# Kernel tuning notes

Measured on AMD Instinct MI355X. Metric: run time of the kernel, lower is better.

## Reference

```python
import jax, jax.numpy as jnp
import numpy as np

B, T, C = 64, 256, 384
H, HD = 6, 64


def setup_inputs() -> dict:
    key = jax.random.key(0)
    ks = jax.random.split(key, 6)
    x = jax.random.normal(ks[0], (B, T, C), dtype=jnp.float32)
    s = 1.0 / np.sqrt(C)
    Wq = jax.random.normal(ks[1], (H, C, HD), dtype=jnp.float32) * s
    Wk = jax.random.normal(ks[2], (H, C, HD), dtype=jnp.float32) * s
    Wv = jax.random.normal(ks[3], (H, C, HD), dtype=jnp.float32) * s
    Wp = jax.random.normal(ks[4], (C, C), dtype=jnp.float32) * s
    bp = jnp.zeros((C,), dtype=jnp.float32)
    return {"x": x, "Wq": Wq, "Wk": Wk, "Wv": Wv, "Wp": Wp, "bp": bp}


def reference(x, Wq, Wk, Wv, Wp, bp):
    # per-head projections (no bias), vectorized over heads
    q = jnp.einsum('btc,hcd->bhtd', x, Wq)
    k = jnp.einsum('btc,hcd->bhtd', x, Wk)
    v = jnp.einsum('btc,hcd->bhtd', x, Wv)
    scale = HD ** (-0.5)
    scores = jnp.einsum('bhtd,bhsd->bhts', q, k) * scale  # [B,H,T,T]
    causal = jnp.tril(jnp.ones((T, T), dtype=bool))
    scores = jnp.where(causal, scores, -jnp.inf)
    wei = jax.nn.softmax(scores, axis=-1)  # dropout is identity in eval mode
    out = jnp.einsum('bhts,bhsd->bhtd', wei, v)
    out = out.transpose(0, 2, 1, 3).reshape(B, T, C)  # concat heads
    return out @ Wp.T + bp
```

## Files before the change

kernel.cpp:

```cpp
#include <hip/hip_runtime.h>
#include <hip/hip_bf16.h>
#include <cstdint>
#include <cstddef>

#define B_ 64
#define T_ 256
#define C_ 384
#define H_ 6
#define HD_ 64

using u16 = unsigned short;
typedef __attribute__((ext_vector_type(8))) short short8;
typedef __attribute__((ext_vector_type(4))) short short4_;
typedef __attribute__((ext_vector_type(4))) float f32x4;

__device__ __forceinline__ u16 f2bf(float f) {
    union { float f; uint32_t u; } x{f};
    uint32_t r = x.u + 0x7fffu + ((x.u >> 16) & 1u);
    return (u16)(r >> 16);
}

__global__ void k_prep(const float* __restrict__ x, const float* __restrict__ Wq,
                       const float* __restrict__ Wk, const float* __restrict__ Wv,
                       const float* __restrict__ Wp, u16* __restrict__ xb,
                       u16* __restrict__ wqkv, u16* __restrict__ wpb) {
    int bid = blockIdx.x;
    if (bid < 3072) {
        int i = (bid * 256 + threadIdx.x) * 8;
        const f32x4* p = (const f32x4*)(x + i);
        f32x4 a = p[0], b = p[1];
        short8 s;
        s[0] = (short)f2bf(a[0]); s[1] = (short)f2bf(a[1]);
        s[2] = (short)f2bf(a[2]); s[3] = (short)f2bf(a[3]);
        s[4] = (short)f2bf(b[0]); s[5] = (short)f2bf(b[1]);
        s[6] = (short)f2bf(b[2]); s[7] = (short)f2bf(b[3]);
        *(short8*)(xb + i) = s;
    } else if (bid < 3180) {
        __shared__ u16 Tt[64 * 65];
        int pb = bid - 3072;
        int which = pb / 36, rem = pb % 36;
        int h = rem / 6, cc0 = (rem % 6) * 64;
        const float* W = (which == 0) ? Wq : ((which == 1) ? Wk : Wv);
        int d = threadIdx.x & 63, cr0 = threadIdx.x >> 6;
#pragma unroll
        for (int p = 0; p < 16; ++p) {
            int cr = p * 4 + cr0;
            Tt[cr * 65 + d] = f2bf(W[(h * 384 + cc0 + cr) * 64 + d]);
        }
        __syncthreads();
        int ccl = threadIdx.x & 63, dl0 = threadIdx.x >> 6;
        int nbase = which * 384 + h * 64;
#pragma unroll
        for (int p = 0; p < 16; ++p) {
            int dl = p * 4 + dl0;
            wqkv[(size_t)(nbase + dl) * 384 + cc0 + ccl] = Tt[ccl * 65 + dl];
        }
    } else {
        int i = ((bid - 3180) * 256 + threadIdx.x) * 8;
        const f32x4* p = (const f32x4*)(Wp + i);
        f32x4 a = p[0], b = p[1];
        short8 s;
        s[0] = (short)f2bf(a[0]); s[1] = (short)f2bf(a[1]);
        s[2] = (short)f2bf(a[2]); s[3] = (short)f2bf(a[3]);
        s[4] = (short)f2bf(b[0]); s[5] = (short)f2bf(b[1]);
        s[6] = (short)f2bf(b[2]); s[7] = (short)f2bf(b[3]);
        *(short8*)(wpb + i) = s;
    }
}

template<int NROWS>
__device__ __forceinline__ void stage_rows(const u16* __restrict__ gbase, int ld,
                                           u16* lds_tile, int wid, int lane, int k0) {
#pragma unroll
    for (int i = 0; i < NROWS / 32; ++i) {
        int chunk = wid * (NROWS / 32) + i;
        int row = chunk * 8 + (lane >> 3);
        int pslot = lane & 7;
        const u16* gp = gbase + (size_t)row * ld + k0 + ((pslot ^ (row & 7)) << 3);
        u16* lp = lds_tile + chunk * 512;
        __builtin_amdgcn_global_load_lds((const __attribute__((address_space(1))) void*)gp,
                                         (__attribute__((address_space(3))) void*)lp, 16, 0, 0);
    }
}

__device__ __forceinline__ void stage_tile(const u16* __restrict__ gbase, int ld,
                                           u16* lds_tile, int wid, int lane, int k0) {
    stage_rows<128>(gbase, ld, lds_tile, wid, lane, k0);
}

__device__ __forceinline__ short8 read_frag(const u16* lds_tile, int row, int ks, int g) {
    int pslot = (ks * 4 + g) ^ (row & 7);
    return *(const short8*)&lds_tile[row * 64 + pslot * 8];
}

#define GEMM_PIPE_LOOP(NT)                                                        \
    int cur = 0;                                                                  \
    for (int t = 0; t < (NT); ++t) {                                              \
        if (t < (NT) - 1) {                                                       \
            stage_tile(Ag, 384, &lds[cur ^ 1][0], wid, lane, (t + 1) * 64);       \
            stage_tile(Bg, 384, &lds[cur ^ 1][8192], wid, lane, (t + 1) * 64);    \
            asm volatile("s_waitcnt vmcnt(8)" ::: "memory");                      \
        } else {                                                                  \
            asm volatile("s_waitcnt vmcnt(0)" ::: "memory");                      \
        }                                                                         \
        __builtin_amdgcn_s_barrier();                                             \
        __builtin_amdgcn_sched_barrier(0);                                        \
        const u16* A = &lds[cur][0];                                              \
        const u16* Bm = &lds[cur][8192];                                          \
        short8 af[2][4], bf[2][4];                                                \
        _Pragma("unroll")                                                         \
        for (int ks = 0; ks < 2; ++ks) {                                          \
            _Pragma("unroll")                                                     \
            for (int mf = 0; mf < 4; ++mf) af[ks][mf] = read_frag(A, wm * 64 + mf * 16 + c, ks, g); \
            _Pragma("unroll")                                                     \
            for (int nf = 0; nf < 4; ++nf) bf[ks][nf] = read_frag(Bm, wn * 64 + nf * 16 + c, ks, g); \
        }                                                                         \
        _Pragma("unroll")                                                         \
        for (int ks = 0; ks < 2; ++ks)                                            \
            _Pragma("unroll")                                                     \
            for (int mf = 0; mf < 4; ++mf)                                        \
                _Pragma("unroll")                                                 \
                for (int nf = 0; nf < 4; ++nf)                                    \
                    acc[mf][nf] = __builtin_amdgcn_mfma_f32_16x16x32_bf16(af[ks][mf], bf[ks][nf], acc[mf][nf], 0, 0, 0); \
        __builtin_amdgcn_sched_barrier(0);                                        \
        __builtin_amdgcn_s_barrier();                                             \
        cur ^= 1;                                                                 \
    }

__global__ __launch_bounds__(256, 2) void k_gemm_qkv(const u16* __restrict__ xb, const u16* __restrict__ wb,
                                                     u16* __restrict__ q, u16* __restrict__ k,
                                                     u16* __restrict__ v) {
    __shared__ alignas(16) u16 lds[2][16384];
    const int tid = threadIdx.x, lane = tid & 63, wid = tid >> 6;
    const int wm = wid >> 1, wn = wid & 1, g = lane >> 4, c = lane & 15;
    const int wg = blockIdx.x;
    const int xcd = wg & 7, q8 = wg >> 3;
    const int mj = (q8 / 9) * 8 + xcd;
    const int nk = q8 % 9;
    const int n0 = nk * 128, m0 = mj * 128;
    const u16* Ag = xb + (size_t)m0 * 384;
    const u16* Bg = wb + (size_t)n0 * 384;
    f32x4 acc[4][4] = {};
    stage_tile(Ag, 384, &lds[0][0], wid, lane, 0);
    stage_tile(Bg, 384, &lds[0][8192], wid, lane, 0);
    GEMM_PIPE_LOOP(6)
    const int which = n0 / 384;
    u16* dst = (which == 0) ? q : ((which == 1) ? k : v);
    const int h = ((n0 + wn * 64) % 384) / 64;
#pragma unroll
    for (int mf = 0; mf < 4; ++mf)
#pragma unroll
        for (int nf = 0; nf < 4; ++nf)
#pragma unroll
            for (int r = 0; r < 4; ++r) {
                int m = m0 + wm * 64 + mf * 16 + g * 4 + r;
                int d = nf * 16 + c;
                int b = m >> 8, t = m & 255;
                dst[((b * H_ + h) * T_ + t) * HD_ + d] = f2bf(acc[mf][nf][r]);
            }
}

__global__ __launch_bounds__(256, 2) void k_attn(const u16* __restrict__ q, const u16* __restrict__ k,
                                                 const u16* __restrict__ v, u16* __restrict__ ao) {
    __shared__ alignas(16) u16 Kl[2][64 * 64];
    __shared__ alignas(16) u16 Vt[2][64][72];
    const int tid = threadIdx.x, bh = blockIdx.x;
    const int lane = tid & 63, wid = tid >> 6;
    const int g = lane >> 4, c = lane & 15;
    const int bq = bh * 256;

    const int vd0 = (tid & 15) * 4;
    const int vs0 = (tid >> 4) * 4;
    const int kb0 = ((vs0 >> 5) << 5) | (((vs0 >> 2) & 3) << 3) | (((vs0 >> 4) & 1) << 2);

    short8 qB[4][2];
#pragma unroll
    for (int qf = 0; qf < 4; ++qf)
#pragma unroll
        for (int ks = 0; ks < 2; ++ks) {
            int t = (qf * 4 + wid) * 16 + c;
            qB[qf][ks] = *(const short8*)&q[(bq + t) * 64 + ks * 32 + g * 8];
        }
    float mrun[4], lrun[4];
#pragma unroll
    for (int i = 0; i < 4; ++i) { mrun[i] = -1e30f; lrun[i] = 0.f; }
    f32x4 o[4][4] = {};

    short4_ vv[4];
    stage_rows<64>(k + (size_t)(bq) * 64, 64, &Kl[0][0], wid, lane, 0);
#pragma unroll
    for (int i = 0; i < 4; ++i)
        vv[i] = *(const short4_*)&v[(size_t)(bq + vs0 + i) * 64 + vd0];
#pragma unroll
    for (int j = 0; j < 4; ++j) {
        short4_ w4;
#pragma unroll
        for (int i = 0; i < 4; ++i) w4[i] = vv[i][j];
        *(short4_*)&Vt[0][vd0 + j][kb0] = w4;
    }
    __syncthreads();

#pragma unroll
    for (int kt = 0; kt < 4; ++kt) {
        const int buf = kt & 1;
        if (kt < 3) {
            stage_rows<64>(k + (size_t)(bq + (kt + 1) * 64) * 64, 64, &Kl[buf ^ 1][0], wid, lane, 0);
#pragma unroll
            for (int i = 0; i < 4; ++i)
                vv[i] = *(const short4_*)&v[(size_t)(bq + (kt + 1) * 64 + vs0 + i) * 64 + vd0];
        }
        {
            f32x4 st[4][4] = {};
            __builtin_amdgcn_s_setprio(1);
#pragma unroll
            for (int ks = 0; ks < 2; ++ks) {
                short8 kA[4];
#pragma unroll
                for (int sf = 0; sf < 4; ++sf)
                    kA[sf] = read_frag(&Kl[buf][0], sf * 16 + c, ks, g);
#pragma unroll
                for (int sf = 0; sf < 4; ++sf)
#pragma unroll
                    for (int qf = kt; qf < 4; ++qf)
                        st[sf][qf] = __builtin_amdgcn_mfma_f32_16x16x32_bf16(kA[sf], qB[qf][ks], st[sf][qf], 0, 0, 0);
            }
            __builtin_amdgcn_s_setprio(0);
            float pm[4];
#pragma unroll
            for (int qf = kt; qf < 4; ++qf) pm[qf] = -1e30f;
#pragma unroll
            for (int sf = 0; sf < 4; ++sf)
#pragma unroll
                for (int qf = kt; qf < 4; ++qf)
#pragma unroll
                    for (int r = 0; r < 4; ++r) {
                        float val = st[sf][qf][r] * 0.125f;
                        if (qf == kt) {
                            if (sf * 16 + g * 4 + r > 16 * wid + c) val = -1e30f;
                        }
                        st[sf][qf][r] = val;
                        pm[qf] = fmaxf(pm[qf], val);
                    }
            float alpha[4];
#pragma unroll
            for (int qf = kt; qf < 4; ++qf) {
                pm[qf] = fmaxf(pm[qf], __shfl_xor(pm[qf], 16));
                pm[qf] = fmaxf(pm[qf], __shfl_xor(pm[qf], 32));
                float mnew = fmaxf(mrun[qf], pm[qf]);
                alpha[qf] = __expf(mrun[qf] - mnew);
                mrun[qf] = mnew;
            }
            short8 pA[4][2];
#pragma unroll
            for (int qf = kt; qf < 4; ++qf) {
                float ls = 0.f;
#pragma unroll
                for (int ks = 0; ks < 2; ++ks) {
                    short8 pa;
#pragma unroll
                    for (int half = 0; half < 2; ++half) {
                        f32x4 sv = st[2 * ks + half][qf];
#pragma unroll
                        for (int r = 0; r < 4; ++r) {
                            float p = __expf(sv[r] - mrun[qf]);
                            ls += p;
                            pa[half * 4 + r] = (short)f2bf(p);
                        }
                    }
                    pA[qf][ks] = pa;
                }
                ls += __shfl_xor(ls, 16);
                ls += __shfl_xor(ls, 32);
                lrun[qf] = lrun[qf] * alpha[qf] + ls;
            }
#pragma unroll
            for (int qf = kt; qf < 4; ++qf)
#pragma unroll
                for (int r = 0; r < 4; ++r) {
                    float aof = __shfl(alpha[qf], g * 4 + r);
#pragma unroll
                    for (int df = 0; df < 4; ++df)
                        o[qf][df][r] *= aof;
                }
            __builtin_amdgcn_s_setprio(1);
#pragma unroll
            for (int ks = 0; ks < 2; ++ks) {
                short8 vB[4];
#pragma unroll
                for (int df = 0; df < 4; ++df)
                    vB[df] = *(short8*)&Vt[buf][df * 16 + c][ks * 32 + g * 8];
#pragma unroll
                for (int qf = kt; qf < 4; ++qf)
#pragma unroll
                    for (int df = 0; df < 4; ++df)
                        o[qf][df] = __builtin_amdgcn_mfma_f32_16x16x32_bf16(pA[qf][ks], vB[df], o[qf][df], 0, 0, 0);
            }
            __builtin_amdgcn_s_setprio(0);
        }
        if (kt < 3) {
#pragma unroll
            for (int j = 0; j < 4; ++j) {
                short4_ w4;
#pragma unroll
                for (int i = 0; i < 4; ++i) w4[i] = vv[i][j];
                *(short4_*)&Vt[buf ^ 1][vd0 + j][kb0] = w4;
            }
        }
        __syncthreads();
    }
    const int bb = bh / H_, hh = bh % H_;
#pragma unroll
    for (int qf = 0; qf < 4; ++qf)
#pragma unroll
        for (int r = 0; r < 4; ++r) {
            float inv = 1.0f / __shfl(lrun[qf], g * 4 + r);
            int t = (qf * 4 + wid) * 16 + g * 4 + r;
#pragma unroll
            for (int df = 0; df < 4; ++df) {
                int d = df * 16 + c;
                ao[((size_t)(bb * T_ + t)) * C_ + hh * 64 + d] = f2bf(o[qf][df][r] * inv);
            }
        }
}

__global__ __launch_bounds__(256, 2) void k_gemm_proj(const u16* __restrict__ ab, const u16* __restrict__ wp,
                                                      const float* __restrict__ bp, float* __restrict__ out) {
    __shared__ alignas(16) u16 lds[2][16384];
    const int tid = threadIdx.x, lane = tid & 63, wid = tid >> 6;
    const int wm = wid >> 1, wn = wid & 1, g = lane >> 4, c = lane & 15;
    const int wg = blockIdx.x;
    const int xcd = wg & 7, q8 = wg >> 3;
    const int mj = (q8 / 3) * 8 + xcd;
    const int nk = q8 % 3;
    const int n0 = nk * 128, m0 = mj * 128;
    const u16* Ag = ab + (size_t)m0 * 384;
    const u16* Bg = wp + (size_t)n0 * 384;
    f32x4 acc[4][4] = {};
    stage_tile(Ag, 384, &lds[0][0], wid, lane, 0);
    stage_tile(Bg, 384, &lds[0][8192], wid, lane, 0);
    GEMM_PIPE_LOOP(6)
#pragma unroll
    for (int mf = 0; mf < 4; ++mf)
#pragma unroll
        for (int nf = 0; nf < 4; ++nf)
#pragma unroll
            for (int r = 0; r < 4; ++r) {
                int m = m0 + wm * 64 + mf * 16 + g * 4 + r;
                int n = n0 + wn * 64 + nf * 16 + c;
                out[(size_t)m * C_ + n] = acc[mf][nf][r] + bp[n];
            }
}


extern "C" void kernel_launch(void* const* d_in, const int* in_sizes, int n_in,
                              void* d_out, int out_size, void* d_ws, size_t ws_size,
                              hipStream_t stream) {
    const float* x  = (const float*)d_in[0];
    const float* Wq = (const float*)d_in[1];
    const float* Wk = (const float*)d_in[2];
    const float* Wv = (const float*)d_in[3];
    const float* Wp = (const float*)d_in[4];
    const float* bp = (const float*)d_in[5];
    float* out = (float*)d_out;

    char* ws = (char*)d_ws;
    u16* xb   = (u16*)(ws);
    u16* wqkv = (u16*)(ws + 12582912);
    u16* wpb  = (u16*)(ws + 13467648);
    u16* qb   = (u16*)(ws + 13762560);
    u16* kb   = (u16*)(ws + 26345472);
    u16* vb   = (u16*)(ws + 38928384);
    u16* ab   = (u16*)(ws + 51511296);

    k_prep<<<3252, 256, 0, stream>>>(x, Wq, Wk, Wv, Wp, xb, wqkv, wpb);
    k_gemm_qkv<<<1152, 256, 0, stream>>>(xb, wqkv, qb, kb, vb);
    k_attn<<<384, 256, 0, stream>>>(qb, kb, vb, ab);
    k_gemm_proj<<<384, 256, 0, stream>>>(ab, wpb, bp, out);
}
```

Measured before the change: 61.87 us.

## Switch QKV and projection GEMMs to single-buffered 256x128 tiles

Both GEMM kernels now compute 256x128 output tiles per block, with each wave owning a 64x128 strip, instead of 128x128 tiles on a 2x2 wave grid. The double-buffered prefetch pipeline is replaced by a single LDS buffer that is loaded and fully waited on each K step. The aim is more operand reuse per LDS fragment and fewer blocks, at the cost of no load/compute overlap, higher accumulator register pressure, and fewer blocks than CUs for the projection GEMM.

```diff
diff --git a/kernel.cpp b/kernel.cpp
--- a/kernel.cpp
+++ b/kernel.cpp
@@ -83,81 +83,66 @@
     }
 }
 
-__device__ __forceinline__ void stage_tile(const u16* __restrict__ gbase, int ld,
-                                           u16* lds_tile, int wid, int lane, int k0) {
-    stage_rows<128>(gbase, ld, lds_tile, wid, lane, k0);
-}
-
 __device__ __forceinline__ short8 read_frag(const u16* lds_tile, int row, int ks, int g) {
     int pslot = (ks * 4 + g) ^ (row & 7);
     return *(const short8*)&lds_tile[row * 64 + pslot * 8];
 }
 
-#define GEMM_PIPE_LOOP(NT)                                                        \
-    int cur = 0;                                                                  \
-    for (int t = 0; t < (NT); ++t) {                                              \
-        if (t < (NT) - 1) {                                                       \
-            stage_tile(Ag, 384, &lds[cur ^ 1][0], wid, lane, (t + 1) * 64);       \
-            stage_tile(Bg, 384, &lds[cur ^ 1][8192], wid, lane, (t + 1) * 64);    \
-            asm volatile("s_waitcnt vmcnt(8)" ::: "memory");                      \
-        } else {                                                                  \
-            asm volatile("s_waitcnt vmcnt(0)" ::: "memory");                      \
-        }                                                                         \
+#define GEMM_LOOP_256x128()                                                       \
+    for (int t = 0; t < 6; ++t) {                                                 \
+        stage_rows<256>(Ag, 384, &lds[0], wid, lane, t * 64);                     \
+        stage_rows<128>(Bg, 384, &lds[16384], wid, lane, t * 64);                 \
+        asm volatile("s_waitcnt vmcnt(0)" ::: "memory");                          \
         __builtin_amdgcn_s_barrier();                                             \
         __builtin_amdgcn_sched_barrier(0);                                        \
-        const u16* A = &lds[cur][0];                                              \
-        const u16* Bm = &lds[cur][8192];                                          \
-        short8 af[2][4], bf[2][4];                                                \
         _Pragma("unroll")                                                         \
         for (int ks = 0; ks < 2; ++ks) {                                          \
+            short8 af[4], bf[8];                                                  \
             _Pragma("unroll")                                                     \
-            for (int mf = 0; mf < 4; ++mf) af[ks][mf] = read_frag(A, wm * 64 + mf * 16 + c, ks, g); \
+            for (int mf = 0; mf < 4; ++mf) af[mf] = read_frag(&lds[0], wid * 64 + mf * 16 + c, ks, g); \
             _Pragma("unroll")                                                     \
-            for (int nf = 0; nf < 4; ++nf) bf[ks][nf] = read_frag(Bm, wn * 64 + nf * 16 + c, ks, g); \
-        }                                                                         \
-        _Pragma("unroll")                                                         \
-        for (int ks = 0; ks < 2; ++ks)                                            \
+            for (int nf = 0; nf < 8; ++nf) bf[nf] = read_frag(&lds[16384], nf * 16 + c, ks, g); \
             _Pragma("unroll")                                                     \
             for (int mf = 0; mf < 4; ++mf)                                        \
                 _Pragma("unroll")                                                 \
-                for (int nf = 0; nf < 4; ++nf)                                    \
-                    acc[mf][nf] = __builtin_amdgcn_mfma_f32_16x16x32_bf16(af[ks][mf], bf[ks][nf], acc[mf][nf], 0, 0, 0); \
+                for (int nf = 0; nf < 8; ++nf)                                    \
+                    acc[mf][nf] = __builtin_amdgcn_mfma_f32_16x16x32_bf16(af[mf], bf[nf], acc[mf][nf], 0, 0, 0); \
+        }                                                                         \
         __builtin_amdgcn_sched_barrier(0);                                        \
         __builtin_amdgcn_s_barrier();                                             \
-        cur ^= 1;                                                                 \
     }
 
 __global__ __launch_bounds__(256, 2) void k_gemm_qkv(const u16* __restrict__ xb, const u16* __restrict__ wb,
                                                      u16* __restrict__ q, u16* __restrict__ k,
                                                      u16* __restrict__ v) {
-    __shared__ alignas(16) u16 lds[2][16384];
+    __shared__ alignas(16) u16 lds[24576];
     const int tid = threadIdx.x, lane = tid & 63, wid = tid >> 6;
-    const int wm = wid >> 1, wn = wid & 1, g = lane >> 4, c = lane & 15;
+    const int g = lane >> 4, c = lane & 15;
     const int wg = blockIdx.x;
     const int xcd = wg & 7, q8 = wg >> 3;
     const int mj = (q8 / 9) * 8 + xcd;
     const int nk = q8 % 9;
-    const int n0 = nk * 128, m0 = mj * 128;
+    const int n0 = nk * 128, m0 = mj * 256;
     const u16* Ag = xb + (size_t)m0 * 384;
     const u16* Bg = wb + (size_t)n0 * 384;
-    f32x4 acc[4][4] = {};
-    stage_tile(Ag, 384, &lds[0][0], wid, lane, 0);
-    stage_tile(Bg, 384, &lds[0][8192], wid, lane, 0);
-    GEMM_PIPE_LOOP(6)
+    f32x4 acc[4][8] = {};
+    GEMM_LOOP_256x128()
     const int which = n0 / 384;
     u16* dst = (which == 0) ? q : ((which == 1) ? k : v);
-    const int h = ((n0 + wn * 64) % 384) / 64;
+    const int cbase = n0 % 384;
 #pragma unroll
     for (int mf = 0; mf < 4; ++mf)
 #pragma unroll
-        for (int nf = 0; nf < 4; ++nf)
+        for (int nf = 0; nf < 8; ++nf) {
+            int col = cbase + nf * 16 + c;
+            int h = col >> 6, d = col & 63;
 #pragma unroll
             for (int r = 0; r < 4; ++r) {
-                int m = m0 + wm * 64 + mf * 16 + g * 4 + r;
-                int d = nf * 16 + c;
+                int m = m0 + wid * 64 + mf * 16 + g * 4 + r;
                 int b = m >> 8, t = m & 255;
                 dst[((b * H_ + h) * T_ + t) * HD_ + d] = f2bf(acc[mf][nf][r]);
             }
+        }
 }
 
 __global__ __launch_bounds__(256, 2) void k_attn(const u16* __restrict__ q, const u16* __restrict__ k,
@@ -325,30 +310,30 @@
 
 __global__ __launch_bounds__(256, 2) void k_gemm_proj(const u16* __restrict__ ab, const u16* __restrict__ wp,
                                                       const float* __restrict__ bp, float* __restrict__ out) {
-    __shared__ alignas(16) u16 lds[2][16384];
+    __shared__ alignas(16) u16 lds[24576];
     const int tid = threadIdx.x, lane = tid & 63, wid = tid >> 6;
-    const int wm = wid >> 1, wn = wid & 1, g = lane >> 4, c = lane & 15;
+    const int g = lane >> 4, c = lane & 15;
     const int wg = blockIdx.x;
     const int xcd = wg & 7, q8 = wg >> 3;
     const int mj = (q8 / 3) * 8 + xcd;
     const int nk = q8 % 3;
-    const int n0 = nk * 128, m0 = mj * 128;
+    const int n0 = nk * 128, m0 = mj * 256;
     const u16* Ag = ab + (size_t)m0 * 384;
     const u16* Bg = wp + (size_t)n0 * 384;
-    f32x4 acc[4][4] = {};
-    stage_tile(Ag, 384, &lds[0][0], wid, lane, 0);
-    stage_tile(Bg, 384, &lds[0][8192], wid, lane, 0);
-    GEMM_PIPE_LOOP(6)
+    f32x4 acc[4][8] = {};
+    GEMM_LOOP_256x128()
 #pragma unroll
     for (int mf = 0; mf < 4; ++mf)
 #pragma unroll
-        for (int nf = 0; nf < 4; ++nf)
+        for (int nf = 0; nf < 8; ++nf) {
+            int n = n0 + nf * 16 + c;
+            float b = bp[n];
 #pragma unroll
             for (int r = 0; r < 4; ++r) {
-                int m = m0 + wm * 64 + mf * 16 + g * 4 + r;
-                int n = n0 + wn * 64 + nf * 16 + c;
-                out[(size_t)m * C_ + n] = acc[mf][nf][r] + bp[n];
-            }
+                int m = m0 + wid * 64 + mf * 16 + g * 4 + r;
+                out[(size_t)m * C_ + n] = acc[mf][nf][r] + b;
+            }
+        }
 }
 
 
@@ -373,7 +358,7 @@
     u16* ab   = (u16*)(ws + 51511296);
 
     k_prep<<<3252, 256, 0, stream>>>(x, Wq, Wk, Wv, Wp, xb, wqkv, wpb);
-    k_gemm_qkv<<<1152, 256, 0, stream>>>(xb, wqkv, qb, kb, vb);
+    k_gemm_qkv<<<576, 256, 0, stream>>>(xb, wqkv, qb, kb, vb);
     k_attn<<<384, 256, 0, stream>>>(qb, kb, vb, ab);
-    k_gemm_proj<<<384, 256, 0, stream>>>(ab, wpb, bp, out);
-}
+    k_gemm_proj<<<192, 256, 0, stream>>>(ab, wpb, bp, out);
+}
```

Result: slower. 69.49 us (+12.3%).

## Fuse fp32-to-bf16 conversion of x into the QKV GEMM loader

Applied to the files above, without the earlier changes.

Drops the separate pass that converts x to bf16 and writes it to workspace. The QKV GEMM now stages fp32 x tiles straight into LDS with 32-wide k-steps and converts fragments to bf16 as it reads them, on a reworked 12-step pipeline. This removes a 12.6 MB write and re-read plus part of the prep launch, at the cost of doubled A-tile bytes in LDS, conversion ALU work inside the GEMM loop, and more barriers per tile. Because every N-tile block re-reads x, global fp32 read traffic for the GEMM grows ninefold over the bf16 path, though most of it should hit cache.

```diff
diff --git a/kernel.cpp b/kernel.cpp
--- a/kernel.cpp
+++ b/kernel.cpp
@@ -20,25 +20,13 @@
     return (u16)(r >> 16);
 }
 
-__global__ void k_prep(const float* __restrict__ x, const float* __restrict__ Wq,
-                       const float* __restrict__ Wk, const float* __restrict__ Wv,
-                       const float* __restrict__ Wp, u16* __restrict__ xb,
-                       u16* __restrict__ wqkv, u16* __restrict__ wpb) {
+__global__ void k_prep_w(const float* __restrict__ Wq, const float* __restrict__ Wk,
+                         const float* __restrict__ Wv, const float* __restrict__ Wp,
+                         u16* __restrict__ wqkv, u16* __restrict__ wpb) {
     int bid = blockIdx.x;
-    if (bid < 3072) {
-        int i = (bid * 256 + threadIdx.x) * 8;
-        const f32x4* p = (const f32x4*)(x + i);
-        f32x4 a = p[0], b = p[1];
-        short8 s;
-        s[0] = (short)f2bf(a[0]); s[1] = (short)f2bf(a[1]);
-        s[2] = (short)f2bf(a[2]); s[3] = (short)f2bf(a[3]);
-        s[4] = (short)f2bf(b[0]); s[5] = (short)f2bf(b[1]);
-        s[6] = (short)f2bf(b[2]); s[7] = (short)f2bf(b[3]);
-        *(short8*)(xb + i) = s;
-    } else if (bid < 3180) {
+    if (bid < 108) {
         __shared__ u16 Tt[64 * 65];
-        int pb = bid - 3072;
-        int which = pb / 36, rem = pb % 36;
+        int which = bid / 36, rem = bid % 36;
         int h = rem / 6, cc0 = (rem % 6) * 64;
         const float* W = (which == 0) ? Wq : ((which == 1) ? Wk : Wv);
         int d = threadIdx.x & 63, cr0 = threadIdx.x >> 6;
@@ -56,7 +44,7 @@
             wqkv[(size_t)(nbase + dl) * 384 + cc0 + ccl] = Tt[ccl * 65 + dl];
         }
     } else {
-        int i = ((bid - 3180) * 256 + threadIdx.x) * 8;
+        int i = ((bid - 108) * 256 + threadIdx.x) * 8;
         const f32x4* p = (const f32x4*)(Wp + i);
         f32x4 a = p[0], b = p[1];
         short8 s;
@@ -91,6 +79,257 @@
 __device__ __forceinline__ short8 read_frag(const u16* lds_tile, int row, int ks, int g) {
     int pslot = (ks * 4 + g) ^ (row & 7);
     return *(const short8*)&lds_tile[row * 64 + pslot * 8];
+}
+
+__device__ __forceinline__ void stage_A32(const float* __restrict__ gbase,
+                                          u16* lds_tile, int wid, int lane, int k0) {
+#pragma unroll
+    for (int i = 0; i < 4; ++i) {
+        int chunk = wid * 4 + i;
+        int row = chunk * 8 + (lane >> 3);
+        int pslot = lane & 7;
+        const float* gp = gbase + (size_t)row * 384 + k0 + ((pslot ^ (row & 7)) << 2);
+        u16* lp = lds_tile + chunk * 512;
+        __builtin_amdgcn_global_load_lds((const __attribute__((address_space(1))) void*)gp,
+                                         (__attribute__((address_space(3))) void*)lp, 16, 0, 0);
+    }
+}
+
+__device__ __forceinline__ short8 read_fragA(const u16* tile, int row, int g) {
+    int s0 = (2 * g) ^ (row & 7);
+    int s1 = (2 * g + 1) ^ (row & 7);
+    f32x4 lo = *(const f32x4*)&tile[row * 64 + s0 * 8];
+    f32x4 hi = *(const f32x4*)&tile[row * 64 + s1 * 8];
+    short8 s;
+#pragma unroll
+    for (int e = 0; e < 4; ++e) {
+        s[e] = (short)f2bf(lo[e]);
+        s[4 + e] = (short)f2bf(hi[e]);
+    }
+    return s;
+}
+
+__global__ __launch_bounds__(256, 2) void k_gemm_qkv(const float* __restrict__ x, const u16* __restrict__ wb,
+                                                     u16* __restrict__ q, u16* __restrict__ k,
+                                                     u16* __restrict__ v) {
+    __shared__ alignas(16) u16 lds[32768];
+    const int tid = threadIdx.x, lane = tid & 63, wid = tid >> 6;
+    const int wm = wid >> 1, wn = wid & 1, g = lane >> 4, c = lane & 15;
+    const int wg = blockIdx.x;
+    const int xcd = wg & 7, q8 = wg >> 3;
+    const int mj = (q8 / 9) * 8 + xcd;
+    const int nk = q8 % 9;
+    const int n0 = nk * 128, m0 = mj * 128;
+    const float* Ag = x + (size_t)m0 * 384;
+    const u16* Bg = wb + (size_t)n0 * 384;
+    f32x4 acc[4][4] = {};
+
+    stage_A32(Ag, &lds[0], wid, lane, 0);
+    stage_rows<128>(Bg, 384, &lds[16384], wid, lane, 0);
+
+    for (int s = 0; s < 12; ++s) {
+        const int t = s >> 1, h = s & 1;
+        if (s < 11)
+            stage_A32(Ag, &lds[((s + 1) & 1) * 8192], wid, lane, (s + 1) * 32);
+        if (h == 0 && t < 5)
+            stage_rows<128>(Bg, 384, &lds[16384 + ((t + 1) & 1) * 8192], wid, lane, (t + 1) * 64);
+        if (s <= 9)       asm volatile("s_waitcnt vmcnt(8)" ::: "memory");
+        else if (s == 10) asm volatile("s_waitcnt vmcnt(4)" ::: "memory");
+        else              asm volatile("s_waitcnt vmcnt(0)" ::: "memory");
+        __builtin_amdgcn_s_barrier();
+        __builtin_amdgcn_sched_barrier(0);
+        const u16* A = &lds[(s & 1) * 8192];
+        const u16* Bm = &lds[16384 + (t & 1) * 8192];
+        short8 af[4], bf[4];
+#pragma unroll
+        for (int mf = 0; mf < 4; ++mf) af[mf] = read_fragA(A, wm * 64 + mf * 16 + c, g);
+#pragma unroll
+        for (int nf = 0; nf < 4; ++nf) bf[nf] = read_frag(Bm, wn * 64 + nf * 16 + c, h, g);
+#pragma unroll
+        for (int mf = 0; mf < 4; ++mf)
+#pragma unroll
+            for (int nf = 0; nf < 4; ++nf)
+                acc[mf][nf] = __builtin_amdgcn_mfma_f32_16x16x32_bf16(af[mf], bf[nf], acc[mf][nf], 0, 0, 0);
+        __builtin_amdgcn_sched_barrier(0);
+        __builtin_amdgcn_s_barrier();
+    }
+    const int which = n0 / 384;
+    u16* dst = (which == 0) ? q : ((which == 1) ? k : v);
+    const int h = ((n0 + wn * 64) % 384) / 64;
+#pragma unroll
+    for (int mf = 0; mf < 4; ++mf)
+#pragma unroll
+        for (int nf = 0; nf < 4; ++nf)
+#pragma unroll
+            for (int r = 0; r < 4; ++r) {
+                int m = m0 + wm * 64 + mf * 16 + g * 4 + r;
+                int d = nf * 16 + c;
+                int b = m >> 8, t = m & 255;
+                dst[((b * H_ + h) * T_ + t) * HD_ + d] = f2bf(acc[mf][nf][r]);
+            }
+}
+
+__global__ __launch_bounds__(256, 2) void k_attn(const u16* __restrict__ q, const u16* __restrict__ k,
+                                                 const u16* __restrict__ v, u16* __restrict__ ao) {
+    __shared__ alignas(16) u16 Kl[2][64 * 64];
+    __shared__ alignas(16) u16 Vt[2][64][72];
+    const int tid = threadIdx.x, bh = blockIdx.x;
+    const int lane = tid & 63, wid = tid >> 6;
+    const int g = lane >> 4, c = lane & 15;
+    const int bq = bh * 256;
+
+    const int vd0 = (tid & 15) * 4;
+    const int vs0 = (tid >> 4) * 4;
+    const int kb0 = ((vs0 >> 5) << 5) | (((vs0 >> 2) & 3) << 3) | (((vs0 >> 4) & 1) << 2);
+
+    short8 qB[4][2];
+#pragma unroll
+    for (int qf = 0; qf < 4; ++qf)
+#pragma unroll
+        for (int ks = 0; ks < 2; ++ks) {
+            int t = (qf * 4 + wid) * 16 + c;
+            qB[qf][ks] = *(const short8*)&q[(bq + t) * 64 + ks * 32 + g * 8];
+        }
+    float mrun[4], lrun[4];
+#pragma unroll
+    for (int i = 0; i < 4; ++i) { mrun[i] = -1e30f; lrun[i] = 0.f; }
+    f32x4 o[4][4] = {};
+
+    short4_ vv[4];
+    stage_rows<64>(k + (size_t)(bq) * 64, 64, &Kl[0][0], wid, lane, 0);
+#pragma unroll
+    for (int i = 0; i < 4; ++i)
+        vv[i] = *(const short4_*)&v[(size_t)(bq + vs0 + i) * 64 + vd0];
+#pragma unroll
+    for (int j = 0; j < 4; ++j) {
+        short4_ w4;
+#pragma unroll
+        for (int i = 0; i < 4; ++i) w4[i] = vv[i][j];
+        *(short4_*)&Vt[0][vd0 + j][kb0] = w4;
+    }
+    __syncthreads();
+
+#pragma unroll
+    for (int kt = 0; kt < 4; ++kt) {
+        const int buf = kt & 1;
+        if (kt < 3) {
+            stage_rows<64>(k + (size_t)(bq + (kt + 1) * 64) * 64, 64, &Kl[buf ^ 1][0], wid, lane, 0);
+#pragma unroll
+            for (int i = 0; i < 4; ++i)
+                vv[i] = *(const short4_*)&v[(size_t)(bq + (kt + 1) * 64 + vs0 + i) * 64 + vd0];
+        }
+        {
+            f32x4 st[4][4] = {};
+            __builtin_amdgcn_s_setprio(1);
+#pragma unroll
+            for (int ks = 0; ks < 2; ++ks) {
+                short8 kA[4];
+#pragma unroll
+                for (int sf = 0; sf < 4; ++sf)
+                    kA[sf] = read_frag(&Kl[buf][0], sf * 16 + c, ks, g);
+#pragma unroll
+                for (int sf = 0; sf < 4; ++sf)
+#pragma unroll
+                    for (int qf = kt; qf < 4; ++qf)
+                        st[sf][qf] = __builtin_amdgcn_mfma_f32_16x16x32_bf16(kA[sf], qB[qf][ks], st[sf][qf], 0, 0, 0);
+            }
+            __builtin_amdgcn_s_setprio(0);
+            float pm[4];
+#pragma unroll
+            for (int qf = kt; qf < 4; ++qf) pm[qf] = -1e30f;
+#pragma unroll
+            for (int sf = 0; sf < 4; ++sf)
+#pragma unroll
+                for (int qf = kt; qf < 4; ++qf)
+#pragma unroll
+                    for (int r = 0; r < 4; ++r) {
+                        float val = st[sf][qf][r] * 0.125f;
+                        if (qf == kt) {
+                            if (sf * 16 + g * 4 + r > 16 * wid + c) val = -1e30f;
+                        }
+                        st[sf][qf][r] = val;
+                        pm[qf] = fmaxf(pm[qf], val);
+                    }
+            float alpha[4];
+#pragma unroll
+            for (int qf = kt; qf < 4; ++qf) {
+                pm[qf] = fmaxf(pm[qf], __shfl_xor(pm[qf], 16));
+                pm[qf] = fmaxf(pm[qf], __shfl_xor(pm[qf], 32));
+                float mnew = fmaxf(mrun[qf], pm[qf]);
+                alpha[qf] = __expf(mrun[qf] - mnew);
+                mrun[qf] = mnew;
+            }
+            short8 pA[4][2];
+#pragma unroll
+            for (int qf = kt; qf < 4; ++qf) {
+                float ls = 0.f;
+#pragma unroll
+                for (int ks = 0; ks < 2; ++ks) {
+                    short8 pa;
+#pragma unroll
+                    for (int half = 0; half < 2; ++half) {
+                        f32x4 sv = st[2 * ks + half][qf];
+#pragma unroll
+                        for (int r = 0; r < 4; ++r) {
+                            float p = __expf(sv[r] - mrun[qf]);
+                            ls += p;
+                            pa[half * 4 + r] = (short)f2bf(p);
+                        }
+                    }
+                    pA[qf][ks] = pa;
+                }
+                ls += __shfl_xor(ls, 16);
+                ls += __shfl_xor(ls, 32);
+                lrun[qf] = lrun[qf] * alpha[qf] + ls;
+            }
+#pragma unroll
+            for (int qf = kt; qf < 4; ++qf)
+#pragma unroll
+                for (int r = 0; r < 4; ++r) {
+                    float aof = __shfl(alpha[qf], g * 4 + r);
+#pragma unroll
+                    for (int df = 0; df < 4; ++df)
+                        o[qf][df][r] *= aof;
+                }
+            __builtin_amdgcn_s_setprio(1);
+#pragma unroll
+            for (int ks = 0; ks < 2; ++ks) {
+                short8 vB[4];
+#pragma unroll
+                for (int df = 0; df < 4; ++df)
+                    vB[df] = *(short8*)&Vt[buf][df * 16 + c][ks * 32 + g * 8];
+#pragma unroll
+                for (int qf = kt; qf < 4; ++qf)
+#pragma unroll
+                    for (int df = 0; df < 4; ++df)
+                        o[qf][df] = __builtin_amdgcn_mfma_f32_16x16x32_bf16(pA[qf][ks], vB[df], o[qf][df], 0, 0, 0);
+            }
+            __builtin_amdgcn_s_setprio(0);
+        }
+        if (kt < 3) {
+#pragma unroll
+            for (int j = 0; j < 4; ++j) {
+                short4_ w4;
+#pragma unroll
+                for (int i = 0; i < 4; ++i) w4[i] = vv[i][j];
+                *(short4_*)&Vt[buf ^ 1][vd0 + j][kb0] = w4;
+            }
+        }
+        __syncthreads();
+    }
+    const int bb = bh / H_, hh = bh % H_;
+#pragma unroll
+    for (int qf = 0; qf < 4; ++qf)
+#pragma unroll
+        for (int r = 0; r < 4; ++r) {
+            float inv = 1.0f / __shfl(lrun[qf], g * 4 + r);
+            int t = (qf * 4 + wid) * 16 + g * 4 + r;
+#pragma unroll
+            for (int df = 0; df < 4; ++df) {
+                int d = df * 16 + c;
+                ao[((size_t)(bb * T_ + t)) * C_ + hh * 64 + d] = f2bf(o[qf][df][r] * inv);
+            }
+        }
 }
 
 #define GEMM_PIPE_LOOP(NT)                                                        \
@@ -127,202 +366,6 @@
         cur ^= 1;                                                                 \
     }
 
-__global__ __launch_bounds__(256, 2) void k_gemm_qkv(const u16* __restrict__ xb, const u16* __restrict__ wb,
-                                                     u16* __restrict__ q, u16* __restrict__ k,
-                                                     u16* __restrict__ v) {
-    __shared__ alignas(16) u16 lds[2][16384];
-    const int tid = threadIdx.x, lane = tid & 63, wid = tid >> 6;
-    const int wm = wid >> 1, wn = wid & 1, g = lane >> 4, c = lane & 15;
-    const int wg = blockIdx.x;
-    const int xcd = wg & 7, q8 = wg >> 3;
-    const int mj = (q8 / 9) * 8 + xcd;
-    const int nk = q8 % 9;
-    const int n0 = nk * 128, m0 = mj * 128;
-    const u16* Ag = xb + (size_t)m0 * 384;
-    const u16* Bg = wb + (size_t)n0 * 384;
-    f32x4 acc[4][4] = {};
-    stage_tile(Ag, 384, &lds[0][0], wid, lane, 0);
-    stage_tile(Bg, 384, &lds[0][8192], wid, lane, 0);
-    GEMM_PIPE_LOOP(6)
-    const int which = n0 / 384;
-    u16* dst = (which == 0) ? q : ((which == 1) ? k : v);
-    const int h = ((n0 + wn * 64) % 384) / 64;
-#pragma unroll
-    for (int mf = 0; mf < 4; ++mf)
-#pragma unroll
-        for (int nf = 0; nf < 4; ++nf)
-#pragma unroll
-            for (int r = 0; r < 4; ++r) {
-                int m = m0 + wm * 64 + mf * 16 + g * 4 + r;
-                int d = nf * 16 + c;
-                int b = m >> 8, t = m & 255;
-                dst[((b * H_ + h) * T_ + t) * HD_ + d] = f2bf(acc[mf][nf][r]);
-            }
-}
-
-__global__ __launch_bounds__(256, 2) void k_attn(const u16* __restrict__ q, const u16* __restrict__ k,
-                                                 const u16* __restrict__ v, u16* __restrict__ ao) {
-    __shared__ alignas(16) u16 Kl[2][64 * 64];
-    __shared__ alignas(16) u16 Vt[2][64][72];
-    const int tid = threadIdx.x, bh = blockIdx.x;
-    const int lane = tid & 63, wid = tid >> 6;
-    const int g = lane >> 4, c = lane & 15;
-    const int bq = bh * 256;
-
-    const int vd0 = (tid & 15) * 4;
-    const int vs0 = (tid >> 4) * 4;
-    const int kb0 = ((vs0 >> 5) << 5) | (((vs0 >> 2) & 3) << 3) | (((vs0 >> 4) & 1) << 2);
-
-    short8 qB[4][2];
-#pragma unroll
-    for (int qf = 0; qf < 4; ++qf)
-#pragma unroll
-        for (int ks = 0; ks < 2; ++ks) {
-            int t = (qf * 4 + wid) * 16 + c;
-            qB[qf][ks] = *(const short8*)&q[(bq + t) * 64 + ks * 32 + g * 8];
-        }
-    float mrun[4], lrun[4];
-#pragma unroll
-    for (int i = 0; i < 4; ++i) { mrun[i] = -1e30f; lrun[i] = 0.f; }
-    f32x4 o[4][4] = {};
-
-    short4_ vv[4];
-    stage_rows<64>(k + (size_t)(bq) * 64, 64, &Kl[0][0], wid, lane, 0);
-#pragma unroll
-    for (int i = 0; i < 4; ++i)
-        vv[i] = *(const short4_*)&v[(size_t)(bq + vs0 + i) * 64 + vd0];
-#pragma unroll
-    for (int j = 0; j < 4; ++j) {
-        short4_ w4;
-#pragma unroll
-        for (int i = 0; i < 4; ++i) w4[i] = vv[i][j];
-        *(short4_*)&Vt[0][vd0 + j][kb0] = w4;
-    }
-    __syncthreads();
-
-#pragma unroll
-    for (int kt = 0; kt < 4; ++kt) {
-        const int buf = kt & 1;
-        if (kt < 3) {
-            stage_rows<64>(k + (size_t)(bq + (kt + 1) * 64) * 64, 64, &Kl[buf ^ 1][0], wid, lane, 0);
-#pragma unroll
-            for (int i = 0; i < 4; ++i)
-                vv[i] = *(const short4_*)&v[(size_t)(bq + (kt + 1) * 64 + vs0 + i) * 64 + vd0];
-        }
-        {
-            f32x4 st[4][4] = {};
-            __builtin_amdgcn_s_setprio(1);
-#pragma unroll
-            for (int ks = 0; ks < 2; ++ks) {
-                short8 kA[4];
-#pragma unroll
-                for (int sf = 0; sf < 4; ++sf)
-                    kA[sf] = read_frag(&Kl[buf][0], sf * 16 + c, ks, g);
-#pragma unroll
-                for (int sf = 0; sf < 4; ++sf)
-#pragma unroll
-                    for (int qf = kt; qf < 4; ++qf)
-                        st[sf][qf] = __builtin_amdgcn_mfma_f32_16x16x32_bf16(kA[sf], qB[qf][ks], st[sf][qf], 0, 0, 0);
-            }
-            __builtin_amdgcn_s_setprio(0);
-            float pm[4];
-#pragma unroll
-            for (int qf = kt; qf < 4; ++qf) pm[qf] = -1e30f;
-#pragma unroll
-            for (int sf = 0; sf < 4; ++sf)
-#pragma unroll
-                for (int qf = kt; qf < 4; ++qf)
-#pragma unroll
-                    for (int r = 0; r < 4; ++r) {
-                        float val = st[sf][qf][r] * 0.125f;
-                        if (qf == kt) {
-                            if (sf * 16 + g * 4 + r > 16 * wid + c) val = -1e30f;
-                        }
-                        st[sf][qf][r] = val;
-                        pm[qf] = fmaxf(pm[qf], val);
-                    }
-            float alpha[4];
-#pragma unroll
-            for (int qf = kt; qf < 4; ++qf) {
-                pm[qf] = fmaxf(pm[qf], __shfl_xor(pm[qf], 16));
-                pm[qf] = fmaxf(pm[qf], __shfl_xor(pm[qf], 32));
-                float mnew = fmaxf(mrun[qf], pm[qf]);
-                alpha[qf] = __expf(mrun[qf] - mnew);
-                mrun[qf] = mnew;
-            }
-            short8 pA[4][2];
-#pragma unroll
-            for (int qf = kt; qf < 4; ++qf) {
-                float ls = 0.f;
-#pragma unroll
-                for (int ks = 0; ks < 2; ++ks) {
-                    short8 pa;
-#pragma unroll
-                    for (int half = 0; half < 2; ++half) {
-                        f32x4 sv = st[2 * ks + half][qf];
-#pragma unroll
-                        for (int r = 0; r < 4; ++r) {
-                            float p = __expf(sv[r] - mrun[qf]);
-                            ls += p;
-                            pa[half * 4 + r] = (short)f2bf(p);
-                        }
-                    }
-                    pA[qf][ks] = pa;
-                }
-                ls += __shfl_xor(ls, 16);
-                ls += __shfl_xor(ls, 32);
-                lrun[qf] = lrun[qf] * alpha[qf] + ls;
-            }
-#pragma unroll
-            for (int qf = kt; qf < 4; ++qf)
-#pragma unroll
-                for (int r = 0; r < 4; ++r) {
-                    float aof = __shfl(alpha[qf], g * 4 + r);
-#pragma unroll
-                    for (int df = 0; df < 4; ++df)
-                        o[qf][df][r] *= aof;
-                }
-            __builtin_amdgcn_s_setprio(1);
-#pragma unroll
-            for (int ks = 0; ks < 2; ++ks) {
-                short8 vB[4];
-#pragma unroll
-                for (int df = 0; df < 4; ++df)
-                    vB[df] = *(short8*)&Vt[buf][df * 16 + c][ks * 32 + g * 8];
-#pragma unroll
-                for (int qf = kt; qf < 4; ++qf)
-#pragma unroll
-                    for (int df = 0; df < 4; ++df)
-                        o[qf][df] = __builtin_amdgcn_mfma_f32_16x16x32_bf16(pA[qf][ks], vB[df], o[qf][df], 0, 0, 0);
-            }
-            __builtin_amdgcn_s_setprio(0);
-        }
-        if (kt < 3) {
-#pragma unroll
-            for (int j = 0; j < 4; ++j) {
-                short4_ w4;
-#pragma unroll
-                for (int i = 0; i < 4; ++i) w4[i] = vv[i][j];
-                *(short4_*)&Vt[buf ^ 1][vd0 + j][kb0] = w4;
-            }
-        }
-        __syncthreads();
-    }
-    const int bb = bh / H_, hh = bh % H_;
-#pragma unroll
-    for (int qf = 0; qf < 4; ++qf)
-#pragma unroll
-        for (int r = 0; r < 4; ++r) {
-            float inv = 1.0f / __shfl(lrun[qf], g * 4 + r);
-            int t = (qf * 4 + wid) * 16 + g * 4 + r;
-#pragma unroll
-            for (int df = 0; df < 4; ++df) {
-                int d = df * 16 + c;
-                ao[((size_t)(bb * T_ + t)) * C_ + hh * 64 + d] = f2bf(o[qf][df][r] * inv);
-            }
-        }
-}
-
 __global__ __launch_bounds__(256, 2) void k_gemm_proj(const u16* __restrict__ ab, const u16* __restrict__ wp,
                                                       const float* __restrict__ bp, float* __restrict__ out) {
     __shared__ alignas(16) u16 lds[2][16384];
@@ -364,16 +407,15 @@
     float* out = (float*)d_out;
 
     char* ws = (char*)d_ws;
-    u16* xb   = (u16*)(ws);
-    u16* wqkv = (u16*)(ws + 12582912);
-    u16* wpb  = (u16*)(ws + 13467648);
-    u16* qb   = (u16*)(ws + 13762560);
-    u16* kb   = (u16*)(ws + 26345472);
-    u16* vb   = (u16*)(ws + 38928384);
-    u16* ab   = (u16*)(ws + 51511296);
-
-    k_prep<<<3252, 256, 0, stream>>>(x, Wq, Wk, Wv, Wp, xb, wqkv, wpb);
-    k_gemm_qkv<<<1152, 256, 0, stream>>>(xb, wqkv, qb, kb, vb);
+    u16* wqkv = (u16*)(ws);
+    u16* wpb  = (u16*)(ws + 884736);
+    u16* qb   = (u16*)(ws + 1179648);
+    u16* kb   = (u16*)(ws + 13762560);
+    u16* vb   = (u16*)(ws + 26345472);
+    u16* ab   = (u16*)(ws + 38928384);
+
+    k_prep_w<<<180, 256, 0, stream>>>(Wq, Wk, Wv, Wp, wqkv, wpb);
+    k_gemm_qkv<<<1152, 256, 0, stream>>>(x, wqkv, qb, kb, vb);
     k_attn<<<384, 256, 0, stream>>>(qb, kb, vb, ab);
     k_gemm_proj<<<384, 256, 0, stream>>>(ab, wpb, bp, out);
 }
```

Measured after the change: 70.27 us. 13.6% more time.
